# Kernel tuning notes

Measured on AMD Instinct MI355X. Metric: run time of the kernel, lower is better.

The kernel has to match this reference:

```python
import jax, jax.numpy as jnp
import numpy as np

DIRECTIONS = [(0, 0), (1, 0), (-1, 0), (0, 1), (0, -1)]  # (dx, dy)
BN_EPS = 1e-5


def shift2d(x, directions=DIRECTIONS):
    # x: (B, C, H, W). Split channels into G groups, roll each spatially,
    # zero out the wrapped-around border (zero_pad mode), then concat.
    C = x.shape[1]
    G = len(directions)
    base = C // G
    sizes = [base] * (G - 1) + [C - base * (G - 1)]
    starts = np.concatenate([[0], np.cumsum(sizes)])
    out = []
    for i, (dx, dy) in enumerate(directions):
        chunk = x[:, starts[i]:starts[i + 1]]
        if dx == 0 and dy == 0:
            out.append(chunk)
            continue
        y = jnp.roll(chunk, shift=(dy, dx), axis=(-2, -1))
        if dy > 0:
            y = y.at[..., :dy, :].set(0.0)
        elif dy < 0:
            y = y.at[..., dy:, :].set(0.0)
        if dx > 0:
            y = y.at[..., :, :dx].set(0.0)
        elif dx < 0:
            y = y.at[..., :, dx:].set(0.0)
        out.append(y)
    return jnp.concatenate(out, axis=1)


def setup_inputs() -> dict:
    key = jax.random.key(0)
    k1, k2, k3, k4 = jax.random.split(key, 4)
    B, Cin, Cout, H, W = 32, 256, 256, 56, 56
    x = jax.random.normal(k1, (B, Cin, H, W), dtype=jnp.float32)
    pw_w = jax.random.normal(k2, (Cout, Cin), dtype=jnp.float32) * (1.0 / np.sqrt(Cin))
    gamma = jnp.ones((Cout,), dtype=jnp.float32)
    beta = jnp.zeros((Cout,), dtype=jnp.float32)
    running_mean = jax.random.normal(k3, (Cout,), dtype=jnp.float32) * 0.1
    running_var = jax.random.uniform(k4, (Cout,), dtype=jnp.float32, minval=0.5, maxval=1.5)
    return {"x": x, "pw_w": pw_w, "gamma": gamma, "beta": beta,
            "running_mean": running_mean, "running_var": running_var}


def reference(x, pw_w, gamma, beta, running_mean, running_var):
    # Shift (parameter-free spatial mixing)
    y = shift2d(x)
    # stride=1 -> down is Identity
    # 1x1 conv (no bias): pointwise channel mixing
    y = jnp.einsum('bchw,oc->bohw', y, pw_w)
    # BatchNorm2d (inference form with running stats) + ReLU
    inv = gamma * jax.lax.rsqrt(running_var + BN_EPS)
    y = y * inv[None, :, None, None] + (beta - running_mean * inv)[None, :, None, None]
    return jax.nn.relu(y)
```

## Files before the change

kernel.cpp:

```cpp
#include <hip/hip_runtime.h>

#define H_ 56
#define W_ 56
#define HW_ 3136
#define CIN_ 256
#define COUT_ 256

typedef __attribute__((ext_vector_type(8))) short short8;
typedef __attribute__((ext_vector_type(4))) float f32x4;

__device__ __forceinline__ int swz(int n) { return ((n ^ (n >> 3)) & 7) << 3; }

__device__ __forceinline__ unsigned short f2bf(float f) {
  union { float f; unsigned int i; } v; v.f = f;
  unsigned int b = v.i + (0x7fffu + ((v.i >> 16) & 1u));
  return (unsigned short)(b >> 16);
}

__global__ __launch_bounds__(256, 2)
void shiftconv_gemm(const float* __restrict__ x,
                    const float* __restrict__ wgt,
                    const float* __restrict__ gamma,
                    const float* __restrict__ beta,
                    const float* __restrict__ rmean,
                    const float* __restrict__ rvar,
                    float* __restrict__ out)
{
  __shared__ unsigned short Alds[128 * 64];
  __shared__ unsigned short Blds[128 * 64];
  __shared__ float bnp[256];

  const int t    = threadIdx.x;
  const int bn   = blockIdx.x;
  const int bm   = blockIdx.y;
  const int lane = t & 63;
  const int wv   = t >> 6;
  const int wm   = wv >> 1;
  const int wn   = wv & 1;
  const int quad = lane >> 4;
  const int l15  = lane & 15;

  if (t < 128) {
    int o = bm * 128 + t;
    float inv = gamma[o] * rsqrtf(rvar[o] + 1e-5f);
    bnp[2 * t]     = inv;
    bnp[2 * t + 1] = beta[o] - rmean[o] * inv;
  }

  const int chunk  = t & 15;
  const int krow   = t >> 4;
  const int nloc0  = chunk * 8;
  const int nglob0 = bn * 128 + nloc0;
  const int bidx   = nglob0 / HW_;
  const int rem    = nglob0 - bidx * HW_;
  const int hh     = rem / W_;
  const int w0     = rem - hh * W_;
  const size_t xb  = (size_t)bidx * CIN_ * HW_;

  const int kc  = t & 7;
  const int am0 = t >> 3;

  f32x4 acc[4][4];
  #pragma unroll
  for (int i = 0; i < 4; ++i)
    #pragma unroll
    for (int j = 0; j < 4; ++j)
      acc[i][j] = (f32x4){0.f, 0.f, 0.f, 0.f};

  for (int k0 = 0; k0 < CIN_; k0 += 64) {
    #pragma unroll
    for (int p = 0; p < 4; ++p) {
      int m = am0 + 32 * p;
      int o = bm * 128 + m;
      const float* src = wgt + (size_t)o * CIN_ + k0 + kc * 8;
      float4 f0 = *(const float4*)(src);
      float4 f1 = *(const float4*)(src + 4);
      union { uint4 v; unsigned short s[8]; } pk;
      pk.s[0] = f2bf(f0.x); pk.s[1] = f2bf(f0.y);
      pk.s[2] = f2bf(f0.z); pk.s[3] = f2bf(f0.w);
      pk.s[4] = f2bf(f1.x); pk.s[5] = f2bf(f1.y);
      pk.s[6] = f2bf(f1.z); pk.s[7] = f2bf(f1.w);
      *(uint4*)(&Alds[m * 64 + ((kc * 8) ^ swz(m))]) = pk.v;
    }
    #pragma unroll
    for (int p = 0; p < 4; ++p) {
      int kk = krow + 16 * p;
      int c  = k0 + kk;
      int dx, dy;
      if (c < 102)      { if (c < 51) { dx = 0; dy = 0; } else { dx = 1; dy = 0; } }
      else if (c < 153) { dx = -1; dy = 0; }
      else if (c < 204) { dx = 0;  dy = 1; }
      else              { dx = 0;  dy = -1; }
      int h2 = hh - dy;
      float vals[8];
      if ((unsigned)h2 < (unsigned)H_) {
        const float* row = x + xb + (size_t)c * HW_ + h2 * W_;
        float4 a = *(const float4*)(row + w0);
        float4 b = *(const float4*)(row + w0 + 4);
        float s[8] = {a.x, a.y, a.z, a.w, b.x, b.y, b.z, b.w};
        if (dx == 0) {
          #pragma unroll
          for (int i = 0; i < 8; ++i) vals[i] = s[i];
        } else if (dx == 1) {
          #pragma unroll
          for (int i = 7; i >= 1; --i) vals[i] = s[i - 1];
          vals[0] = (w0 > 0) ? row[w0 - 1] : 0.0f;
        } else {
          #pragma unroll
          for (int i = 0; i < 7; ++i) vals[i] = s[i + 1];
          vals[7] = (w0 + 8 < W_) ? row[w0 + 8] : 0.0f;
        }
      } else {
        #pragma unroll
        for (int i = 0; i < 8; ++i) vals[i] = 0.0f;
      }
      #pragma unroll
      for (int i = 0; i < 8; ++i) {
        int nl = nloc0 + i;
        Blds[nl * 64 + (kk ^ swz(nl))] = f2bf(vals[i]);
      }
    }
    __syncthreads();
    #pragma unroll
    for (int ks = 0; ks < 2; ++ks) {
      int kb = ks * 32 + quad * 8;
      short8 af[4], bf[4];
      #pragma unroll
      for (int f = 0; f < 4; ++f) {
        int ml = wm * 64 + f * 16 + l15;
        af[f] = *(const short8*)(&Alds[ml * 64 + (kb ^ swz(ml))]);
        int nl = wn * 64 + f * 16 + l15;
        bf[f] = *(const short8*)(&Blds[nl * 64 + (kb ^ swz(nl))]);
      }
      #pragma unroll
      for (int mf = 0; mf < 4; ++mf)
        #pragma unroll
        for (int nf = 0; nf < 4; ++nf)
          acc[mf][nf] = __builtin_amdgcn_mfma_f32_16x16x32_bf16(
              af[mf], bf[nf], acc[mf][nf], 0, 0, 0);
    }
    __syncthreads();
  }

  size_t nbase[4];
  #pragma unroll
  for (int nf = 0; nf < 4; ++nf) {
    int ng  = bn * 128 + wn * 64 + nf * 16 + l15;
    int b2  = ng / HW_;
    int hw2 = ng - b2 * HW_;
    nbase[nf] = (size_t)b2 * COUT_ * HW_ + hw2;
  }
  #pragma unroll
  for (int mf = 0; mf < 4; ++mf) {
    int mloc = wm * 64 + mf * 16 + quad * 4;
    float inv[4], add[4];
    #pragma unroll
    for (int r = 0; r < 4; ++r) {
      inv[r] = bnp[2 * (mloc + r)];
      add[r] = bnp[2 * (mloc + r) + 1];
    }
    size_t obase = (size_t)(bm * 128 + mloc) * HW_;
    #pragma unroll
    for (int nf = 0; nf < 4; ++nf) {
      #pragma unroll
      for (int r = 0; r < 4; ++r) {
        float v = acc[mf][nf][r] * inv[r] + add[r];
        out[nbase[nf] + obase + (size_t)r * HW_] = fmaxf(v, 0.0f);
      }
    }
  }
}

extern "C" void kernel_launch(void* const* d_in, const int* in_sizes, int n_in,
                              void* d_out, int out_size, void* d_ws, size_t ws_size,
                              hipStream_t stream) {
  const float* x     = (const float*)d_in[0];
  const float* wgt   = (const float*)d_in[1];
  const float* gamma = (const float*)d_in[2];
  const float* beta  = (const float*)d_in[3];
  const float* rmean = (const float*)d_in[4];
  const float* rvar  = (const float*)d_in[5];
  float* out = (float*)d_out;
  dim3 grid(784, 2);
  shiftconv_gemm<<<grid, dim3(256), 0, stream>>>(x, wgt, gamma, beta, rmean, rvar, out);
}
```

Before: 220.9 us.

## Pre-swizzle bf16 weights in prep kernel and double-buffer LDS with register prefetch

A new prep kernel converts the weights once to bf16, already laid out in the swizzled LDS tile order, and computes the BN scale and shift into workspace. The main kernel copies weight tiles straight into LDS and prefetches the next K-stage of weights and shifted activations into registers while the MFMAs run on a double-buffered LDS. Activation staging is also changed to 4-wide n per thread with 16-byte LDS stores instead of scalar stores. The cost is an extra kernel launch, more registers per thread and twice the shared memory, which may lower occupancy. A fallback kernel is kept for when the workspace is too small.

Result: slower. 235.5 us (+6.6%).

```diff
diff --git a/kernel.cpp b/kernel.cpp
--- a/kernel.cpp
+++ b/kernel.cpp
@@ -8,27 +8,50 @@
 
 typedef __attribute__((ext_vector_type(8))) short short8;
 typedef __attribute__((ext_vector_type(4))) float f32x4;
+typedef unsigned short ushort_t;
 
 __device__ __forceinline__ int swz(int n) { return ((n ^ (n >> 3)) & 7) << 3; }
 
-__device__ __forceinline__ unsigned short f2bf(float f) {
+__device__ __forceinline__ ushort_t f2bf(float f) {
   union { float f; unsigned int i; } v; v.f = f;
   unsigned int b = v.i + (0x7fffu + ((v.i >> 16) & 1u));
-  return (unsigned short)(b >> 16);
+  return (ushort_t)(b >> 16);
+}
+
+__device__ __forceinline__ void cdir(int c, int& dx, int& dy) {
+  if (c < 102)      { if (c < 51) { dx = 0; dy = 0; } else { dx = 1; dy = 0; } }
+  else if (c < 153) { dx = -1; dy = 0; }
+  else if (c < 204) { dx = 0;  dy = 1; }
+  else              { dx = 0;  dy = -1; }
+}
+
+__global__ void prep_kernel(const float* __restrict__ wgt, const float* __restrict__ gamma,
+                            const float* __restrict__ beta, const float* __restrict__ rmean,
+                            const float* __restrict__ rvar,
+                            ushort_t* __restrict__ wsw, float* __restrict__ bnp) {
+  int idx = blockIdx.x * 256 + threadIdx.x;
+  int tile = idx >> 13;
+  int within = idx & 8191;
+  int m = within >> 6;
+  int off = within & 63;
+  int j = off >> 3, klo = off & 7;
+  int koct = j ^ ((m ^ (m >> 3)) & 7);
+  int bm = tile >> 2, s = tile & 3;
+  int o = bm * 128 + m;
+  int c = s * 64 + koct * 8 + klo;
+  wsw[idx] = f2bf(wgt[o * CIN_ + c]);
+  if (idx < COUT_) {
+    float inv = gamma[idx] * rsqrtf(rvar[idx] + 1e-5f);
+    bnp[2 * idx]     = inv;
+    bnp[2 * idx + 1] = beta[idx] - rmean[idx] * inv;
+  }
 }
 
 __global__ __launch_bounds__(256, 2)
-void shiftconv_gemm(const float* __restrict__ x,
-                    const float* __restrict__ wgt,
-                    const float* __restrict__ gamma,
-                    const float* __restrict__ beta,
-                    const float* __restrict__ rmean,
-                    const float* __restrict__ rvar,
-                    float* __restrict__ out)
-{
-  __shared__ unsigned short Alds[128 * 64];
-  __shared__ unsigned short Blds[128 * 64];
-  __shared__ float bnp[256];
+void shiftconv_mfma(const float* __restrict__ x, const ushort_t* __restrict__ wsw,
+                    const float* __restrict__ bnp, float* __restrict__ out) {
+  __shared__ ushort_t Ab[2][8192];
+  __shared__ ushort_t Bb[2][8192];
 
   const int t    = threadIdx.x;
   const int bn   = blockIdx.x;
@@ -40,25 +63,63 @@
   const int quad = lane >> 4;
   const int l15  = lane & 15;
 
-  if (t < 128) {
-    int o = bm * 128 + t;
-    float inv = gamma[o] * rsqrtf(rvar[o] + 1e-5f);
-    bnp[2 * t]     = inv;
-    bnp[2 * t + 1] = beta[o] - rmean[o] * inv;
-  }
-
-  const int chunk  = t & 15;
-  const int krow   = t >> 4;
-  const int nloc0  = chunk * 8;
-  const int nglob0 = bn * 128 + nloc0;
-  const int bidx   = nglob0 / HW_;
-  const int rem    = nglob0 - bidx * HW_;
-  const int hh     = rem / W_;
-  const int w0     = rem - hh * W_;
-  const size_t xb  = (size_t)bidx * CIN_ * HW_;
-
-  const int kc  = t & 7;
-  const int am0 = t >> 3;
+  const int nq = t & 31;
+  const int kb = t >> 5;
+  const int n0 = bn * 128 + nq * 4;
+  const int bidx = n0 / HW_;
+  const int rem  = n0 - bidx * HW_;
+  const int hh   = rem / W_;
+  const int w0   = rem - hh * W_;
+  const float* xb = x + (size_t)bidx * CIN_ * HW_;
+
+  const ushort_t* wtile = wsw + (size_t)(bm * 4) * 8192;
+
+  uint4  areg[4];
+  float4 bmain[8];
+  float  bedge[8];
+
+  #define LOAD_A(s)                                                         \
+    { const ushort_t* src = wtile + (s) * 8192 + t * 8;                     \
+      _Pragma("unroll")                                                     \
+      for (int r = 0; r < 4; ++r) areg[r] = *(const uint4*)(src + r * 2048); }
+
+  #define LOAD_B(s)                                                         \
+    { _Pragma("unroll")                                                     \
+      for (int j = 0; j < 8; ++j) {                                         \
+        int c = (s) * 64 + kb * 8 + j;                                      \
+        int dx, dy; cdir(c, dx, dy);                                        \
+        int h2 = hh - dy;                                                   \
+        if ((unsigned)h2 < (unsigned)H_) {                                  \
+          const float* row = xb + (size_t)c * HW_ + h2 * W_;                \
+          bmain[j] = *(const float4*)(row + w0);                            \
+          bedge[j] = (dx == 1) ? ((w0 > 0) ? row[w0 - 1] : 0.f)             \
+                   : (dx == -1) ? ((w0 < 52) ? row[w0 + 4] : 0.f) : 0.f;    \
+        } else { bmain[j] = make_float4(0.f,0.f,0.f,0.f); bedge[j] = 0.f; } \
+      } }
+
+  #define STAGE(buf, s)                                                     \
+    { _Pragma("unroll")                                                     \
+      for (int r = 0; r < 4; ++r)                                           \
+        *(uint4*)&Ab[buf][r * 2048 + t * 8] = areg[r];                      \
+      _Pragma("unroll")                                                     \
+      for (int i = 0; i < 4; ++i) {                                         \
+        int n = nq * 4 + i;                                                 \
+        ushort_t kv[8];                                                     \
+        _Pragma("unroll")                                                   \
+        for (int j = 0; j < 8; ++j) {                                       \
+          int c = (s) * 64 + kb * 8 + j;                                    \
+          int dx, dy; cdir(c, dx, dy);                                      \
+          float v;                                                          \
+          if (dx == 0)      v = ((const float*)&bmain[j])[i];               \
+          else if (dx == 1) v = (i == 0) ? bedge[j]                         \
+                                         : ((const float*)&bmain[j])[i - 1];\
+          else              v = (i == 3) ? bedge[j]                         \
+                                         : ((const float*)&bmain[j])[i + 1];\
+          kv[j] = f2bf(v);                                                  \
+        }                                                                   \
+        *(uint4*)&Bb[buf][n * 64 + ((kb ^ ((n ^ (n >> 3)) & 7)) << 3)] =    \
+            *(uint4*)kv;                                                    \
+      } }
 
   f32x4 acc[4][4];
   #pragma unroll
@@ -67,79 +128,33 @@
     for (int j = 0; j < 4; ++j)
       acc[i][j] = (f32x4){0.f, 0.f, 0.f, 0.f};
 
-  for (int k0 = 0; k0 < CIN_; k0 += 64) {
-    #pragma unroll
-    for (int p = 0; p < 4; ++p) {
-      int m = am0 + 32 * p;
-      int o = bm * 128 + m;
-      const float* src = wgt + (size_t)o * CIN_ + k0 + kc * 8;
-      float4 f0 = *(const float4*)(src);
-      float4 f1 = *(const float4*)(src + 4);
-      union { uint4 v; unsigned short s[8]; } pk;
-      pk.s[0] = f2bf(f0.x); pk.s[1] = f2bf(f0.y);
-      pk.s[2] = f2bf(f0.z); pk.s[3] = f2bf(f0.w);
-      pk.s[4] = f2bf(f1.x); pk.s[5] = f2bf(f1.y);
-      pk.s[6] = f2bf(f1.z); pk.s[7] = f2bf(f1.w);
-      *(uint4*)(&Alds[m * 64 + ((kc * 8) ^ swz(m))]) = pk.v;
-    }
-    #pragma unroll
-    for (int p = 0; p < 4; ++p) {
-      int kk = krow + 16 * p;
-      int c  = k0 + kk;
-      int dx, dy;
-      if (c < 102)      { if (c < 51) { dx = 0; dy = 0; } else { dx = 1; dy = 0; } }
-      else if (c < 153) { dx = -1; dy = 0; }
-      else if (c < 204) { dx = 0;  dy = 1; }
-      else              { dx = 0;  dy = -1; }
-      int h2 = hh - dy;
-      float vals[8];
-      if ((unsigned)h2 < (unsigned)H_) {
-        const float* row = x + xb + (size_t)c * HW_ + h2 * W_;
-        float4 a = *(const float4*)(row + w0);
-        float4 b = *(const float4*)(row + w0 + 4);
-        float s[8] = {a.x, a.y, a.z, a.w, b.x, b.y, b.z, b.w};
-        if (dx == 0) {
-          #pragma unroll
-          for (int i = 0; i < 8; ++i) vals[i] = s[i];
-        } else if (dx == 1) {
-          #pragma unroll
-          for (int i = 7; i >= 1; --i) vals[i] = s[i - 1];
-          vals[0] = (w0 > 0) ? row[w0 - 1] : 0.0f;
-        } else {
-          #pragma unroll
-          for (int i = 0; i < 7; ++i) vals[i] = s[i + 1];
-          vals[7] = (w0 + 8 < W_) ? row[w0 + 8] : 0.0f;
-        }
-      } else {
-        #pragma unroll
-        for (int i = 0; i < 8; ++i) vals[i] = 0.0f;
-      }
-      #pragma unroll
-      for (int i = 0; i < 8; ++i) {
-        int nl = nloc0 + i;
-        Blds[nl * 64 + (kk ^ swz(nl))] = f2bf(vals[i]);
-      }
-    }
+  LOAD_A(0);
+  LOAD_B(0);
+
+  #pragma unroll
+  for (int s = 0; s < 4; ++s) {
+    const int buf = s & 1;
+    STAGE(buf, s);
     __syncthreads();
+    if (s < 3) { LOAD_A(s + 1); LOAD_B(s + 1); }
     #pragma unroll
     for (int ks = 0; ks < 2; ++ks) {
-      int kb = ks * 32 + quad * 8;
-      short8 af[4], bf[4];
+      int kb8 = ks * 32 + quad * 8;
+      short8 af[4], bfr[4];
       #pragma unroll
       for (int f = 0; f < 4; ++f) {
         int ml = wm * 64 + f * 16 + l15;
-        af[f] = *(const short8*)(&Alds[ml * 64 + (kb ^ swz(ml))]);
+        af[f]  = *(const short8*)(&Ab[buf][ml * 64 + (kb8 ^ swz(ml))]);
         int nl = wn * 64 + f * 16 + l15;
-        bf[f] = *(const short8*)(&Blds[nl * 64 + (kb ^ swz(nl))]);
+        bfr[f] = *(const short8*)(&Bb[buf][nl * 64 + (kb8 ^ swz(nl))]);
       }
       #pragma unroll
       for (int mf = 0; mf < 4; ++mf)
         #pragma unroll
         for (int nf = 0; nf < 4; ++nf)
           acc[mf][nf] = __builtin_amdgcn_mfma_f32_16x16x32_bf16(
-              af[mf], bf[nf], acc[mf][nf], 0, 0, 0);
-    }
-    __syncthreads();
+              af[mf], bfr[nf], acc[mf][nf], 0, 0, 0);
+    }
   }
 
   size_t nbase[4];
@@ -153,13 +168,14 @@
   #pragma unroll
   for (int mf = 0; mf < 4; ++mf) {
     int mloc = wm * 64 + mf * 16 + quad * 4;
+    int og   = bm * 128 + mloc;
     float inv[4], add[4];
     #pragma unroll
     for (int r = 0; r < 4; ++r) {
-      inv[r] = bnp[2 * (mloc + r)];
-      add[r] = bnp[2 * (mloc + r) + 1];
-    }
-    size_t obase = (size_t)(bm * 128 + mloc) * HW_;
+      inv[r] = bnp[2 * (og + r)];
+      add[r] = bnp[2 * (og + r) + 1];
+    }
+    size_t obase = (size_t)og * HW_;
     #pragma unroll
     for (int nf = 0; nf < 4; ++nf) {
       #pragma unroll
@@ -168,6 +184,110 @@
         out[nbase[nf] + obase + (size_t)r * HW_] = fmaxf(v, 0.0f);
       }
     }
+  }
+}
+
+__global__ __launch_bounds__(256, 2)
+void shiftconv_gemm_fb(const float* __restrict__ x, const float* __restrict__ wgt,
+                       const float* __restrict__ gamma, const float* __restrict__ beta,
+                       const float* __restrict__ rmean, const float* __restrict__ rvar,
+                       float* __restrict__ out) {
+  __shared__ ushort_t Alds[128 * 64];
+  __shared__ ushort_t Blds[128 * 64];
+  __shared__ float bnp[256];
+  const int t = threadIdx.x, bn = blockIdx.x, bm = blockIdx.y;
+  const int lane = t & 63, wv = t >> 6, wm = wv >> 1, wn = wv & 1;
+  const int quad = lane >> 4, l15 = lane & 15;
+  if (t < 128) {
+    int o = bm * 128 + t;
+    float inv = gamma[o] * rsqrtf(rvar[o] + 1e-5f);
+    bnp[2 * t] = inv; bnp[2 * t + 1] = beta[o] - rmean[o] * inv;
+  }
+  const int chunk = t & 15, krow = t >> 4;
+  const int nloc0 = chunk * 8, nglob0 = bn * 128 + nloc0;
+  const int bidx = nglob0 / HW_, rem = nglob0 - bidx * HW_;
+  const int hh = rem / W_, w0 = rem - hh * W_;
+  const size_t xb = (size_t)bidx * CIN_ * HW_;
+  const int kc = t & 7, am0 = t >> 3;
+  f32x4 acc[4][4];
+  #pragma unroll
+  for (int i = 0; i < 4; ++i)
+    #pragma unroll
+    for (int j = 0; j < 4; ++j) acc[i][j] = (f32x4){0.f,0.f,0.f,0.f};
+  for (int k0 = 0; k0 < CIN_; k0 += 64) {
+    #pragma unroll
+    for (int p = 0; p < 4; ++p) {
+      int m = am0 + 32 * p, o = bm * 128 + m;
+      const float* src = wgt + (size_t)o * CIN_ + k0 + kc * 8;
+      float4 f0 = *(const float4*)(src); float4 f1 = *(const float4*)(src + 4);
+      union { uint4 v; ushort_t s[8]; } pk;
+      pk.s[0]=f2bf(f0.x); pk.s[1]=f2bf(f0.y); pk.s[2]=f2bf(f0.z); pk.s[3]=f2bf(f0.w);
+      pk.s[4]=f2bf(f1.x); pk.s[5]=f2bf(f1.y); pk.s[6]=f2bf(f1.z); pk.s[7]=f2bf(f1.w);
+      *(uint4*)(&Alds[m * 64 + ((kc * 8) ^ swz(m))]) = pk.v;
+    }
+    #pragma unroll
+    for (int p = 0; p < 4; ++p) {
+      int kk = krow + 16 * p, c = k0 + kk;
+      int dx, dy; cdir(c, dx, dy);
+      int h2 = hh - dy;
+      float vals[8];
+      if ((unsigned)h2 < (unsigned)H_) {
+        const float* row = x + xb + (size_t)c * HW_ + h2 * W_;
+        float4 a = *(const float4*)(row + w0); float4 b = *(const float4*)(row + w0 + 4);
+        float sArr[8] = {a.x,a.y,a.z,a.w,b.x,b.y,b.z,b.w};
+        if (dx == 0) { for (int i = 0; i < 8; ++i) vals[i] = sArr[i]; }
+        else if (dx == 1) { for (int i = 7; i >= 1; --i) vals[i] = sArr[i-1];
+                            vals[0] = (w0 > 0) ? row[w0 - 1] : 0.f; }
+        else { for (int i = 0; i < 7; ++i) vals[i] = sArr[i+1];
+               vals[7] = (w0 + 8 < W_) ? row[w0 + 8] : 0.f; }
+      } else { for (int i = 0; i < 8; ++i) vals[i] = 0.f; }
+      #pragma unroll
+      for (int i = 0; i < 8; ++i) {
+        int nl = nloc0 + i;
+        Blds[nl * 64 + (kk ^ swz(nl))] = f2bf(vals[i]);
+      }
+    }
+    __syncthreads();
+    #pragma unroll
+    for (int ks = 0; ks < 2; ++ks) {
+      int kb8 = ks * 32 + quad * 8;
+      short8 af[4], bfr[4];
+      #pragma unroll
+      for (int f = 0; f < 4; ++f) {
+        int ml = wm * 64 + f * 16 + l15;
+        af[f] = *(const short8*)(&Alds[ml * 64 + (kb8 ^ swz(ml))]);
+        int nl = wn * 64 + f * 16 + l15;
+        bfr[f] = *(const short8*)(&Blds[nl * 64 + (kb8 ^ swz(nl))]);
+      }
+      #pragma unroll
+      for (int mf = 0; mf < 4; ++mf)
+        #pragma unroll
+        for (int nf = 0; nf < 4; ++nf)
+          acc[mf][nf] = __builtin_amdgcn_mfma_f32_16x16x32_bf16(af[mf], bfr[nf], acc[mf][nf], 0, 0, 0);
+    }
+    __syncthreads();
+  }
+  size_t nbase[4];
+  #pragma unroll
+  for (int nf = 0; nf < 4; ++nf) {
+    int ng = bn * 128 + wn * 64 + nf * 16 + l15;
+    int b2 = ng / HW_, hw2 = ng - b2 * HW_;
+    nbase[nf] = (size_t)b2 * COUT_ * HW_ + hw2;
+  }
+  #pragma unroll
+  for (int mf = 0; mf < 4; ++mf) {
+    int mloc = wm * 64 + mf * 16 + quad * 4;
+    float inv[4], add[4];
+    #pragma unroll
+    for (int r = 0; r < 4; ++r) { inv[r] = bnp[2*(mloc+r)]; add[r] = bnp[2*(mloc+r)+1]; }
+    size_t obase = (size_t)(bm * 128 + mloc) * HW_;
+    #pragma unroll
+    for (int nf = 0; nf < 4; ++nf)
+      #pragma unroll
+      for (int r = 0; r < 4; ++r) {
+        float v = acc[mf][nf][r] * inv[r] + add[r];
+        out[nbase[nf] + obase + (size_t)r * HW_] = fmaxf(v, 0.0f);
+      }
   }
 }
 
@@ -182,5 +302,12 @@
   const float* rvar  = (const float*)d_in[5];
   float* out = (float*)d_out;
   dim3 grid(784, 2);
-  shiftconv_gemm<<<grid, dim3(256), 0, stream>>>(x, wgt, gamma, beta, rmean, rvar, out);
-}
+  if (ws_size >= (size_t)(131072 + 2048)) {
+    ushort_t* wsw = (ushort_t*)d_ws;
+    float* bnp = (float*)((char*)d_ws + 131072);
+    prep_kernel<<<256, 256, 0, stream>>>(wgt, gamma, beta, rmean, rvar, wsw, bnp);
+    shiftconv_mfma<<<grid, dim3(256), 0, stream>>>(x, wsw, bnp, out);
+  } else {
+    shiftconv_gemm_fb<<<grid, dim3(256), 0, stream>>>(x, wgt, gamma, beta, rmean, rvar, out);
+  }
+}
```
